# Optimization experiments

Measured on AMD Instinct MI355X. Metric: run time of the kernel, lower is better.

## Reference

```python
import jax, jax.numpy as jnp
import numpy as np

B, L, D = 4096, 50, 64
U, V, R = 100000, 100000, 5

def _lin(key, fan_out, fan_in):
    kw, kb = jax.random.split(key)
    s = 1.0 / np.sqrt(fan_in)
    return (jax.random.uniform(kw, (fan_out, fan_in), jnp.float32, -s, s),
            jax.random.uniform(kb, (fan_out,), jnp.float32, -s, s))

def setup_inputs() -> dict:
    key = jax.random.key(0)
    ks = jax.random.split(key, 12)
    w_r1_w, w_r1_b = _lin(ks[0], D, 2 * D)
    w_r2_w, w_r2_b = _lin(ks[1], D, D)
    att1_w, att1_b = _lin(ks[2], D, 2 * D)
    att2_w, att2_b = _lin(ks[3], D, D)
    att3_w, att3_b = _lin(ks[4], 1, D)
    return {
        "nodes": jax.random.randint(ks[5], (B,), 0, U),
        "history_uv": jax.random.randint(ks[6], (B, L), 0, V),
        "history_r": jax.random.randint(ks[7], (B, L), 0, R),
        "history_uvt": jax.random.randint(ks[8], (B, L), 0, 512),
        "v2e_w": jax.random.normal(ks[9], (V, D), jnp.float32) * 0.05,
        "u2e_w": jax.random.normal(ks[10], (U, D), jnp.float32) * 0.05,
        "r2e_w": jax.random.normal(ks[11], (R, D), jnp.float32) * 0.05,
        "w_r1_w": w_r1_w, "w_r1_b": w_r1_b,
        "w_r2_w": w_r2_w, "w_r2_b": w_r2_b,
        "att1_w": att1_w, "att1_b": att1_b,
        "att2_w": att2_w, "att2_b": att2_b,
        "att3_w": att3_w, "att3_b": att3_b,
    }

def reference(nodes, history_uv, history_r, history_uvt,
              v2e_w, u2e_w, r2e_w,
              w_r1_w, w_r1_b, w_r2_w, w_r2_b,
              att1_w, att1_b, att2_w, att2_b, att3_w, att3_b):
    # Gathers (uv=True branch): item embeddings for neighbor history, user rep for node
    e_uv = v2e_w[history_uv]          # (B, L, D)
    e_r = r2e_w[history_r]            # (B, L, D)
    uv_rep = u2e_w[nodes]             # (B, D)
    # Two-layer MLP on [e_uv ; e_r]
    x = jnp.concatenate([e_uv, e_r], axis=-1)               # (B, L, 2D)
    h = jax.nn.relu(jnp.einsum('blk,dk->bld', x, w_r1_w) + w_r1_b)
    o = jax.nn.relu(jnp.einsum('blk,dk->bld', h, w_r2_w) + w_r2_b)  # (B, L, D)
    # GraphRec Attention: MLP([o ; uv_rep]) -> scalar -> softmax over neighbors
    uv_b = jnp.broadcast_to(uv_rep[:, None, :], o.shape)     # (B, L, D)
    xa = jnp.concatenate([o, uv_b], axis=-1)                 # (B, L, 2D)
    a = jax.nn.relu(jnp.einsum('blk,dk->bld', xa, att1_w) + att1_b)
    a = jax.nn.relu(jnp.einsum('blk,dk->bld', a, att2_w) + att2_b)
    s = jnp.einsum('bld,od->blo', a, att3_w)[..., 0] + att3_b[0]    # (B, L)
    w = jax.nn.softmax(s, axis=1)                            # softmax over neighbors
    # att_history = o^T @ att_w  per node
    out = jnp.einsum('bld,bl->bd', o, w)                     # (B, D)
    return out
```

## Files before the change

kernel.cpp:

```cpp
#include <hip/hip_runtime.h>


#define LNB 50

typedef _Float16 f16x8 __attribute__((ext_vector_type(8)));
typedef float    f32x4 __attribute__((ext_vector_type(4)));

__device__ __forceinline__ int swz(int r, int bytecol) {
  return (r * 128 + bytecol) ^ ((r & 7) << 4);
}

__device__ __forceinline__ f16x8 cvt8(const float* __restrict__ p) {
  const float4 lo = *(const float4*)p;
  const float4 hi = *(const float4*)(p + 4);
  f16x8 a;
  a[0] = (_Float16)lo.x; a[1] = (_Float16)lo.y;
  a[2] = (_Float16)lo.z; a[3] = (_Float16)lo.w;
  a[4] = (_Float16)hi.x; a[5] = (_Float16)hi.y;
  a[6] = (_Float16)hi.z; a[7] = (_Float16)hi.w;
  return a;
}

__global__ void prep_weights(const float* __restrict__ w1, const float* __restrict__ w2,
                             const float* __restrict__ a1, const float* __restrict__ a2,
                             _Float16* __restrict__ wf) {
  int i = blockIdx.x * 256 + threadIdx.x;
  if (i < 8192) wf[i]         = (_Float16)w1[i];
  if (i < 4096) wf[8192 + i]  = (_Float16)w2[i];
  if (i < 8192) wf[12288 + i] = (_Float16)a1[i];
  if (i < 4096) wf[20480 + i] = (_Float16)a2[i];
}

__global__ __launch_bounds__(64, 4) void mlp_kernel(
    const int* __restrict__ hist_uv,
    const int* __restrict__ hist_r,
    const float* __restrict__ v2e,
    const float* __restrict__ r2e,
    const float* __restrict__ b1,
    const float* __restrict__ b2,
    const _Float16* __restrict__ wf,
    _Float16* __restrict__ ows) {
  __shared__ _Float16 T[64 * 64];
  const int lane = threadIdx.x;
  const int lr = lane & 15;
  const int kq = lane >> 4;
  const int r0 = blockIdx.x * 64;

  const _Float16* w1f = wf;
  const _Float16* w2f = wf + 8192;

  {
    f16x8 Bf[4][4];
#pragma unroll
    for (int kt = 0; kt < 4; ++kt)
#pragma unroll
      for (int nt = 0; nt < 4; ++nt)
        Bf[kt][nt] = *(const f16x8*)(w1f + (nt * 16 + lr) * 128 + kt * 32 + kq * 8);

    float bias1[4];
#pragma unroll
    for (int nt = 0; nt < 4; ++nt) bias1[nt] = b1[nt * 16 + lr];

#pragma unroll
    for (int m = 0; m < 4; ++m) {
      const int r = r0 + m * 16 + lr;
      const int iu = hist_uv[r];
      const int ir = hist_r[r];
      const float* pu = v2e + (size_t)iu * 64;
      const float* pr = r2e + (size_t)ir * 64;
      f16x8 A[4];
      A[0] = cvt8(pu + kq * 8);
      A[1] = cvt8(pu + 32 + kq * 8);
      A[2] = cvt8(pr + kq * 8);
      A[3] = cvt8(pr + 32 + kq * 8);
#pragma unroll
      for (int nt = 0; nt < 4; ++nt) {
        f32x4 acc = {0.f, 0.f, 0.f, 0.f};
#pragma unroll
        for (int kt = 0; kt < 4; ++kt)
          acc = __builtin_amdgcn_mfma_f32_16x16x32_f16(A[kt], Bf[kt][nt], acc, 0, 0, 0);
        const int c = nt * 16 + lr;
#pragma unroll
        for (int j = 0; j < 4; ++j) {
          const int row = m * 16 + kq * 4 + j;
          const float v = fmaxf(acc[j] + bias1[nt], 0.f);
          *(_Float16*)((char*)T + swz(row, 2 * c)) = (_Float16)v;
        }
      }
    }
  }
  __syncthreads();

  {
    f16x8 Bf[2][4];
#pragma unroll
    for (int kt = 0; kt < 2; ++kt)
#pragma unroll
      for (int nt = 0; nt < 4; ++nt)
        Bf[kt][nt] = *(const f16x8*)(w2f + (nt * 16 + lr) * 64 + kt * 32 + kq * 8);

    float bias2[4];
#pragma unroll
    for (int nt = 0; nt < 4; ++nt) bias2[nt] = b2[nt * 16 + lr];

#pragma unroll
    for (int m = 0; m < 4; ++m) {
      const int r = m * 16 + lr;
      f16x8 A0  = *(const f16x8*)((char*)T + swz(r, 2 * (kq * 8)));
      f16x8 A1v = *(const f16x8*)((char*)T + swz(r, 2 * (32 + kq * 8)));
      f32x4 accs[4];
#pragma unroll
      for (int nt = 0; nt < 4; ++nt) {
        f32x4 acc = {0.f, 0.f, 0.f, 0.f};
        acc = __builtin_amdgcn_mfma_f32_16x16x32_f16(A0,  Bf[0][nt], acc, 0, 0, 0);
        acc = __builtin_amdgcn_mfma_f32_16x16x32_f16(A1v, Bf[1][nt], acc, 0, 0, 0);
        accs[nt] = acc;
      }
      asm volatile("s_waitcnt lgkmcnt(0)" ::: "memory");
#pragma unroll
      for (int nt = 0; nt < 4; ++nt) {
        const int c = nt * 16 + lr;
#pragma unroll
        for (int j = 0; j < 4; ++j) {
          const int row = m * 16 + kq * 4 + j;
          const float v = fmaxf(accs[nt][j] + bias2[nt], 0.f);
          *(_Float16*)((char*)T + swz(row, 2 * c)) = (_Float16)v;
        }
      }
    }
  }
  __syncthreads();

  {
    char* dst = (char*)ows + (size_t)r0 * 128;
#pragma unroll
    for (int p = 0; p < 8; ++p) {
      const int idx = p * 1024 + lane * 16;
      f16x8 v = *(const f16x8*)((const char*)T + swz(idx >> 7, idx & 127));
      *(f16x8*)(dst + idx) = v;
    }
  }
}

__global__ __launch_bounds__(64, 4) void att_kernel(
    const int* __restrict__ nodes,
    const float* __restrict__ u2e,
    const float* __restrict__ ab1,
    const float* __restrict__ ab2,
    const float* __restrict__ a3w,
    const _Float16* __restrict__ wf,
    const _Float16* __restrict__ ows,
    float* __restrict__ out) {
  __shared__ _Float16 T[64 * 64];
  __shared__ float sc[64];
  __shared__ float wt[64];
  const int lane = threadIdx.x;
  const int lr = lane & 15;
  const int kq = lane >> 4;
  const int b = blockIdx.x;
  const int node = nodes[b];

  const _Float16* a1f = wf + 12288;
  const _Float16* a2f = wf + 20480;
  const _Float16* ob = ows + (size_t)b * LNB * 64;

  {
    f16x8 Bf[4][4];
#pragma unroll
    for (int kt = 0; kt < 4; ++kt)
#pragma unroll
      for (int nt = 0; nt < 4; ++nt)
        Bf[kt][nt] = *(const f16x8*)(a1f + (nt * 16 + lr) * 128 + kt * 32 + kq * 8);

    const f16x8 U2 = cvt8(u2e + (size_t)node * 64 + kq * 8);
    const f16x8 U3 = cvt8(u2e + (size_t)node * 64 + 32 + kq * 8);

    float biasa1[4];
#pragma unroll
    for (int nt = 0; nt < 4; ++nt) biasa1[nt] = ab1[nt * 16 + lr];

#pragma unroll
    for (int m = 0; m < 4; ++m) {
      const int r = m * 16 + lr;
      f16x8 A0, A1v;
      if (r < LNB) {
        const _Float16* orow = ob + (size_t)r * 64;
        A0  = *(const f16x8*)(orow + kq * 8);
        A1v = *(const f16x8*)(orow + 32 + kq * 8);
      } else {
#pragma unroll
        for (int i = 0; i < 8; ++i) { A0[i] = (_Float16)0.f; A1v[i] = (_Float16)0.f; }
      }
#pragma unroll
      for (int nt = 0; nt < 4; ++nt) {
        f32x4 acc = {0.f, 0.f, 0.f, 0.f};
        acc = __builtin_amdgcn_mfma_f32_16x16x32_f16(A0,  Bf[0][nt], acc, 0, 0, 0);
        acc = __builtin_amdgcn_mfma_f32_16x16x32_f16(A1v, Bf[1][nt], acc, 0, 0, 0);
        acc = __builtin_amdgcn_mfma_f32_16x16x32_f16(U2,  Bf[2][nt], acc, 0, 0, 0);
        acc = __builtin_amdgcn_mfma_f32_16x16x32_f16(U3,  Bf[3][nt], acc, 0, 0, 0);
        const int c = nt * 16 + lr;
#pragma unroll
        for (int j = 0; j < 4; ++j) {
          const int row = m * 16 + kq * 4 + j;
          const float v = fmaxf(acc[j] + biasa1[nt], 0.f);
          *(_Float16*)((char*)T + swz(row, 2 * c)) = (_Float16)v;
        }
      }
    }
  }
  __syncthreads();

  {
    f16x8 Bf[2][4];
#pragma unroll
    for (int kt = 0; kt < 2; ++kt)
#pragma unroll
      for (int nt = 0; nt < 4; ++nt)
        Bf[kt][nt] = *(const f16x8*)(a2f + (nt * 16 + lr) * 64 + kt * 32 + kq * 8);

    float biasa2[4], a3c[4];
#pragma unroll
    for (int nt = 0; nt < 4; ++nt) {
      biasa2[nt] = ab2[nt * 16 + lr];
      a3c[nt] = a3w[nt * 16 + lr];
    }

#pragma unroll
    for (int m = 0; m < 4; ++m) {
      const int r = m * 16 + lr;
      f16x8 A0  = *(const f16x8*)((char*)T + swz(r, 2 * (kq * 8)));
      f16x8 A1v = *(const f16x8*)((char*)T + swz(r, 2 * (32 + kq * 8)));
      float part[4] = {0.f, 0.f, 0.f, 0.f};
#pragma unroll
      for (int nt = 0; nt < 4; ++nt) {
        f32x4 acc = {0.f, 0.f, 0.f, 0.f};
        acc = __builtin_amdgcn_mfma_f32_16x16x32_f16(A0,  Bf[0][nt], acc, 0, 0, 0);
        acc = __builtin_amdgcn_mfma_f32_16x16x32_f16(A1v, Bf[1][nt], acc, 0, 0, 0);
#pragma unroll
        for (int j = 0; j < 4; ++j) {
          const float v = fmaxf(acc[j] + biasa2[nt], 0.f);
          part[j] += v * a3c[nt];
        }
      }
#pragma unroll
      for (int mask = 1; mask < 16; mask <<= 1)
#pragma unroll
        for (int j = 0; j < 4; ++j) part[j] += __shfl_xor(part[j], mask);
      if (lr == 0) {
#pragma unroll
        for (int j = 0; j < 4; ++j) sc[m * 16 + kq * 4 + j] = part[j];
      }
    }
  }
  __syncthreads();

  {
    float sv = (lane < LNB) ? sc[lane] : -1e30f;
    float mx = sv;
#pragma unroll
    for (int mask = 1; mask < 64; mask <<= 1) mx = fmaxf(mx, __shfl_xor(mx, mask));
    const float e = __expf(sv - mx);
    float s = e;
#pragma unroll
    for (int mask = 1; mask < 64; mask <<= 1) s += __shfl_xor(s, mask);
    wt[lane] = e / s;
  }
  __syncthreads();

  {
    float acc = 0.f;
    const _Float16* oc = ob + lane;
#pragma unroll
    for (int l = 0; l < LNB; ++l) acc += wt[l] * (float)oc[(size_t)l * 64];
    out[(size_t)b * 64 + lane] = acc;
  }
}

extern "C" void kernel_launch(void* const* d_in, const int* in_sizes, int n_in,
                              void* d_out, int out_size, void* d_ws, size_t ws_size,
                              hipStream_t stream) {
  (void)in_sizes; (void)n_in; (void)out_size; (void)ws_size;
  const int* nodes = (const int*)d_in[0];
  const int* huv   = (const int*)d_in[1];
  const int* hr    = (const int*)d_in[2];
  const float* v2e = (const float*)d_in[4];
  const float* u2e = (const float*)d_in[5];
  const float* r2e = (const float*)d_in[6];
  const float* w1  = (const float*)d_in[7];
  const float* b1  = (const float*)d_in[8];
  const float* w2  = (const float*)d_in[9];
  const float* b2  = (const float*)d_in[10];
  const float* a1  = (const float*)d_in[11];
  const float* ab1 = (const float*)d_in[12];
  const float* a2  = (const float*)d_in[13];
  const float* ab2 = (const float*)d_in[14];
  const float* a3  = (const float*)d_in[15];

  _Float16* wf  = (_Float16*)d_ws;
  _Float16* ows = (_Float16*)((char*)d_ws + 65536);

  prep_weights<<<32, 256, 0, stream>>>(w1, w2, a1, a2, wf);
  mlp_kernel<<<3200, 64, 0, stream>>>(huv, hr, v2e, r2e, b1, b2, wf, ows);
  att_kernel<<<4096, 64, 0, stream>>>(nodes, u2e, ab1, ab2, a3, wf, ows,
                                      (float*)d_out);
}
```

Measured before the change: 162.3 us.

## Fuse MLP, attention and weighted sum into one per-batch kernel

The separate weight-prep, MLP and attention kernels become one kernel with one block per batch row. The o tiles stay in registers and LDS instead of making a round trip through global memory. The uv_rep part of att1 is computed once per block and reused as the accumulator start, and the final weighted sum is done from register fragments with shuffles. The cost is that each block now converts the fp32 weights to fp16 itself, and 14 of the 64 rows are padded compute per block. The kernel also uses more registers, which may lower occupancy.

New measurement: 198.5 us. 22.3% more time.

```diff
diff --git a/kernel.cpp b/kernel.cpp
--- a/kernel.cpp
+++ b/kernel.cpp
@@ -21,33 +21,30 @@
   return a;
 }
 
-__global__ void prep_weights(const float* __restrict__ w1, const float* __restrict__ w2,
-                             const float* __restrict__ a1, const float* __restrict__ a2,
-                             _Float16* __restrict__ wf) {
-  int i = blockIdx.x * 256 + threadIdx.x;
-  if (i < 8192) wf[i]         = (_Float16)w1[i];
-  if (i < 4096) wf[8192 + i]  = (_Float16)w2[i];
-  if (i < 8192) wf[12288 + i] = (_Float16)a1[i];
-  if (i < 4096) wf[20480 + i] = (_Float16)a2[i];
-}
-
-__global__ __launch_bounds__(64, 4) void mlp_kernel(
+__global__ __launch_bounds__(64, 4) void uvagg_fused(
+    const int* __restrict__ nodes,
     const int* __restrict__ hist_uv,
     const int* __restrict__ hist_r,
     const float* __restrict__ v2e,
+    const float* __restrict__ u2e,
     const float* __restrict__ r2e,
+    const float* __restrict__ w1,
     const float* __restrict__ b1,
+    const float* __restrict__ w2,
     const float* __restrict__ b2,
-    const _Float16* __restrict__ wf,
-    _Float16* __restrict__ ows) {
+    const float* __restrict__ a1,
+    const float* __restrict__ ab1,
+    const float* __restrict__ a2,
+    const float* __restrict__ ab2,
+    const float* __restrict__ a3w,
+    float* __restrict__ out) {
   __shared__ _Float16 T[64 * 64];
+  __shared__ float scb[64];
+  __shared__ float wtb[64];
   const int lane = threadIdx.x;
   const int lr = lane & 15;
   const int kq = lane >> 4;
-  const int r0 = blockIdx.x * 64;
-
-  const _Float16* w1f = wf;
-  const _Float16* w2f = wf + 8192;
+  const int b = blockIdx.x;
 
   {
     f16x8 Bf[4][4];
@@ -55,7 +52,7 @@
     for (int kt = 0; kt < 4; ++kt)
 #pragma unroll
       for (int nt = 0; nt < 4; ++nt)
-        Bf[kt][nt] = *(const f16x8*)(w1f + (nt * 16 + lr) * 128 + kt * 32 + kq * 8);
+        Bf[kt][nt] = cvt8(w1 + (nt * 16 + lr) * 128 + kt * 32 + kq * 8);
 
     float bias1[4];
 #pragma unroll
@@ -63,9 +60,9 @@
 
 #pragma unroll
     for (int m = 0; m < 4; ++m) {
-      const int r = r0 + m * 16 + lr;
-      const int iu = hist_uv[r];
-      const int ir = hist_r[r];
+      const int rr = b * LNB + (m * 16 + lr < LNB ? m * 16 + lr : LNB - 1);
+      const int iu = hist_uv[rr];
+      const int ir = hist_r[rr];
       const float* pu = v2e + (size_t)iu * 64;
       const float* pr = r2e + (size_t)ir * 64;
       f16x8 A[4];
@@ -91,13 +88,22 @@
   }
   __syncthreads();
 
+  f16x8 HA0[4], HA1[4];
+#pragma unroll
+  for (int m = 0; m < 4; ++m) {
+    const int r = m * 16 + lr;
+    HA0[m] = *(const f16x8*)((char*)T + swz(r, 2 * (kq * 8)));
+    HA1[m] = *(const f16x8*)((char*)T + swz(r, 2 * (32 + kq * 8)));
+  }
+  __syncthreads();
+
   {
     f16x8 Bf[2][4];
 #pragma unroll
     for (int kt = 0; kt < 2; ++kt)
 #pragma unroll
       for (int nt = 0; nt < 4; ++nt)
-        Bf[kt][nt] = *(const f16x8*)(w2f + (nt * 16 + lr) * 64 + kt * 32 + kq * 8);
+        Bf[kt][nt] = cvt8(w2 + (nt * 16 + lr) * 64 + kt * 32 + kq * 8);
 
     float bias2[4];
 #pragma unroll
@@ -105,25 +111,16 @@
 
 #pragma unroll
     for (int m = 0; m < 4; ++m) {
-      const int r = m * 16 + lr;
-      f16x8 A0  = *(const f16x8*)((char*)T + swz(r, 2 * (kq * 8)));
-      f16x8 A1v = *(const f16x8*)((char*)T + swz(r, 2 * (32 + kq * 8)));
-      f32x4 accs[4];
 #pragma unroll
       for (int nt = 0; nt < 4; ++nt) {
         f32x4 acc = {0.f, 0.f, 0.f, 0.f};
-        acc = __builtin_amdgcn_mfma_f32_16x16x32_f16(A0,  Bf[0][nt], acc, 0, 0, 0);
-        acc = __builtin_amdgcn_mfma_f32_16x16x32_f16(A1v, Bf[1][nt], acc, 0, 0, 0);
-        accs[nt] = acc;
-      }
-      asm volatile("s_waitcnt lgkmcnt(0)" ::: "memory");
-#pragma unroll
-      for (int nt = 0; nt < 4; ++nt) {
+        acc = __builtin_amdgcn_mfma_f32_16x16x32_f16(HA0[m], Bf[0][nt], acc, 0, 0, 0);
+        acc = __builtin_amdgcn_mfma_f32_16x16x32_f16(HA1[m], Bf[1][nt], acc, 0, 0, 0);
         const int c = nt * 16 + lr;
 #pragma unroll
         for (int j = 0; j < 4; ++j) {
           const int row = m * 16 + kq * 4 + j;
-          const float v = fmaxf(accs[nt][j] + bias2[nt], 0.f);
+          const float v = fmaxf(acc[j] + bias2[nt], 0.f);
           *(_Float16*)((char*)T + swz(row, 2 * c)) = (_Float16)v;
         }
       }
@@ -131,49 +128,42 @@
   }
   __syncthreads();
 
-  {
-    char* dst = (char*)ows + (size_t)r0 * 128;
-#pragma unroll
-    for (int p = 0; p < 8; ++p) {
-      const int idx = p * 1024 + lane * 16;
-      f16x8 v = *(const f16x8*)((const char*)T + swz(idx >> 7, idx & 127));
-      *(f16x8*)(dst + idx) = v;
-    }
-  }
-}
-
-__global__ __launch_bounds__(64, 4) void att_kernel(
-    const int* __restrict__ nodes,
-    const float* __restrict__ u2e,
-    const float* __restrict__ ab1,
-    const float* __restrict__ ab2,
-    const float* __restrict__ a3w,
-    const _Float16* __restrict__ wf,
-    const _Float16* __restrict__ ows,
-    float* __restrict__ out) {
-  __shared__ _Float16 T[64 * 64];
-  __shared__ float sc[64];
-  __shared__ float wt[64];
-  const int lane = threadIdx.x;
-  const int lr = lane & 15;
-  const int kq = lane >> 4;
-  const int b = blockIdx.x;
-  const int node = nodes[b];
-
-  const _Float16* a1f = wf + 12288;
-  const _Float16* a2f = wf + 20480;
-  const _Float16* ob = ows + (size_t)b * LNB * 64;
-
-  {
-    f16x8 Bf[4][4];
-#pragma unroll
-    for (int kt = 0; kt < 4; ++kt)
+  f16x8 OA0[4], OA1[4];
+#pragma unroll
+  for (int m = 0; m < 4; ++m) {
+    const int r = m * 16 + lr;
+    OA0[m] = *(const f16x8*)((char*)T + swz(r, 2 * (kq * 8)));
+    OA1[m] = *(const f16x8*)((char*)T + swz(r, 2 * (32 + kq * 8)));
+  }
+  __syncthreads();
+
+  {
+    const int node = nodes[b];
+    f32x4 acc_u[4];
+    {
+      f16x8 Bu[2][4];
+#pragma unroll
+      for (int kt = 0; kt < 2; ++kt)
+#pragma unroll
+        for (int nt = 0; nt < 4; ++nt)
+          Bu[kt][nt] = cvt8(a1 + (nt * 16 + lr) * 128 + (kt + 2) * 32 + kq * 8);
+      const f16x8 U2 = cvt8(u2e + (size_t)node * 64 + kq * 8);
+      const f16x8 U3 = cvt8(u2e + (size_t)node * 64 + 32 + kq * 8);
+#pragma unroll
+      for (int nt = 0; nt < 4; ++nt) {
+        f32x4 acc = {0.f, 0.f, 0.f, 0.f};
+        acc = __builtin_amdgcn_mfma_f32_16x16x32_f16(U2, Bu[0][nt], acc, 0, 0, 0);
+        acc = __builtin_amdgcn_mfma_f32_16x16x32_f16(U3, Bu[1][nt], acc, 0, 0, 0);
+        acc_u[nt] = acc;
+      }
+    }
+
+    f16x8 Bf[2][4];
+#pragma unroll
+    for (int kt = 0; kt < 2; ++kt)
 #pragma unroll
       for (int nt = 0; nt < 4; ++nt)
-        Bf[kt][nt] = *(const f16x8*)(a1f + (nt * 16 + lr) * 128 + kt * 32 + kq * 8);
-
-    const f16x8 U2 = cvt8(u2e + (size_t)node * 64 + kq * 8);
-    const f16x8 U3 = cvt8(u2e + (size_t)node * 64 + 32 + kq * 8);
+        Bf[kt][nt] = cvt8(a1 + (nt * 16 + lr) * 128 + kt * 32 + kq * 8);
 
     float biasa1[4];
 #pragma unroll
@@ -181,23 +171,11 @@
 
 #pragma unroll
     for (int m = 0; m < 4; ++m) {
-      const int r = m * 16 + lr;
-      f16x8 A0, A1v;
-      if (r < LNB) {
-        const _Float16* orow = ob + (size_t)r * 64;
-        A0  = *(const f16x8*)(orow + kq * 8);
-        A1v = *(const f16x8*)(orow + 32 + kq * 8);
-      } else {
-#pragma unroll
-        for (int i = 0; i < 8; ++i) { A0[i] = (_Float16)0.f; A1v[i] = (_Float16)0.f; }
-      }
-#pragma unroll
-      for (int nt = 0; nt < 4; ++nt) {
-        f32x4 acc = {0.f, 0.f, 0.f, 0.f};
-        acc = __builtin_amdgcn_mfma_f32_16x16x32_f16(A0,  Bf[0][nt], acc, 0, 0, 0);
-        acc = __builtin_amdgcn_mfma_f32_16x16x32_f16(A1v, Bf[1][nt], acc, 0, 0, 0);
-        acc = __builtin_amdgcn_mfma_f32_16x16x32_f16(U2,  Bf[2][nt], acc, 0, 0, 0);
-        acc = __builtin_amdgcn_mfma_f32_16x16x32_f16(U3,  Bf[3][nt], acc, 0, 0, 0);
+#pragma unroll
+      for (int nt = 0; nt < 4; ++nt) {
+        f32x4 acc = acc_u[nt];
+        acc = __builtin_amdgcn_mfma_f32_16x16x32_f16(OA0[m], Bf[0][nt], acc, 0, 0, 0);
+        acc = __builtin_amdgcn_mfma_f32_16x16x32_f16(OA1[m], Bf[1][nt], acc, 0, 0, 0);
         const int c = nt * 16 + lr;
 #pragma unroll
         for (int j = 0; j < 4; ++j) {
@@ -216,7 +194,7 @@
     for (int kt = 0; kt < 2; ++kt)
 #pragma unroll
       for (int nt = 0; nt < 4; ++nt)
-        Bf[kt][nt] = *(const f16x8*)(a2f + (nt * 16 + lr) * 64 + kt * 32 + kq * 8);
+        Bf[kt][nt] = cvt8(a2 + (nt * 16 + lr) * 64 + kt * 32 + kq * 8);
 
     float biasa2[4], a3c[4];
 #pragma unroll
@@ -248,14 +226,14 @@
         for (int j = 0; j < 4; ++j) part[j] += __shfl_xor(part[j], mask);
       if (lr == 0) {
 #pragma unroll
-        for (int j = 0; j < 4; ++j) sc[m * 16 + kq * 4 + j] = part[j];
-      }
-    }
-  }
-  __syncthreads();
-
-  {
-    float sv = (lane < LNB) ? sc[lane] : -1e30f;
+        for (int j = 0; j < 4; ++j) scb[m * 16 + kq * 4 + j] = part[j];
+      }
+    }
+  }
+  __syncthreads();
+
+  {
+    float sv = (lane < LNB) ? scb[lane] : -1e30f;
     float mx = sv;
 #pragma unroll
     for (int mask = 1; mask < 64; mask <<= 1) mx = fmaxf(mx, __shfl_xor(mx, mask));
@@ -263,23 +241,47 @@
     float s = e;
 #pragma unroll
     for (int mask = 1; mask < 64; mask <<= 1) s += __shfl_xor(s, mask);
-    wt[lane] = e / s;
-  }
-  __syncthreads();
-
-  {
-    float acc = 0.f;
-    const _Float16* oc = ob + lane;
-#pragma unroll
-    for (int l = 0; l < LNB; ++l) acc += wt[l] * (float)oc[(size_t)l * 64];
-    out[(size_t)b * 64 + lane] = acc;
-  }
+    wtb[lane] = (lane < LNB) ? (e / s) : 0.f;
+  }
+  __syncthreads();
+
+  {
+    float wrow[4];
+#pragma unroll
+    for (int m = 0; m < 4; ++m) wrow[m] = wtb[m * 16 + lr];
+
+    float p0[8] = {0,0,0,0,0,0,0,0};
+    float p1[8] = {0,0,0,0,0,0,0,0};
+#pragma unroll
+    for (int m = 0; m < 4; ++m)
+#pragma unroll
+      for (int i = 0; i < 8; ++i) {
+        p0[i] += wrow[m] * (float)OA0[m][i];
+        p1[i] += wrow[m] * (float)OA1[m][i];
+      }
+#pragma unroll
+    for (int mask = 1; mask < 16; mask <<= 1)
+#pragma unroll
+      for (int i = 0; i < 8; ++i) {
+        p0[i] += __shfl_xor(p0[i], mask);
+        p1[i] += __shfl_xor(p1[i], mask);
+      }
+    if (lr == 0) {
+#pragma unroll
+      for (int i = 0; i < 8; ++i) {
+        scb[kq * 8 + i] = p0[i];
+        scb[32 + kq * 8 + i] = p1[i];
+      }
+    }
+  }
+  __syncthreads();
+  out[(size_t)b * 64 + lane] = scb[lane];
 }
 
 extern "C" void kernel_launch(void* const* d_in, const int* in_sizes, int n_in,
                               void* d_out, int out_size, void* d_ws, size_t ws_size,
                               hipStream_t stream) {
-  (void)in_sizes; (void)n_in; (void)out_size; (void)ws_size;
+  (void)in_sizes; (void)n_in; (void)out_size; (void)d_ws; (void)ws_size;
   const int* nodes = (const int*)d_in[0];
   const int* huv   = (const int*)d_in[1];
   const int* hr    = (const int*)d_in[2];
@@ -296,11 +298,7 @@
   const float* ab2 = (const float*)d_in[14];
   const float* a3  = (const float*)d_in[15];
 
-  _Float16* wf  = (_Float16*)d_ws;
-  _Float16* ows = (_Float16*)((char*)d_ws + 65536);
-
-  prep_weights<<<32, 256, 0, stream>>>(w1, w2, a1, a2, wf);
-  mlp_kernel<<<3200, 64, 0, stream>>>(huv, hr, v2e, r2e, b1, b2, wf, ows);
-  att_kernel<<<4096, 64, 0, stream>>>(nodes, u2e, ab1, ab2, a3, wf, ows,
-                                      (float*)d_out);
+  uvagg_fused<<<4096, 64, 0, stream>>>(nodes, huv, hr, v2e, u2e, r2e,
+                                       w1, b1, w2, b2, a1, ab1, a2, ab2, a3,
+                                       (float*)d_out);
 }
```
